# Kernel optimization log

Measured on AMD Instinct MI355X. Metric: run time of the kernel, lower is better.

## Reference

```python
import jax, jax.numpy as jnp
import numpy as np

N = 100000      # nodes
E = 1600000     # edges
DIN = 128       # input_dim
DH = 128        # hidden_dim
DOUT = 64       # output_dim
NL = 10         # num_label_layers


def setup_inputs() -> dict:
    key = jax.random.key(0)
    ks = jax.random.split(key, 12)
    x = jax.random.normal(ks[0], (N, DIN), jnp.float32)
    y = jax.random.uniform(ks[1], (N, DOUT), jnp.float32)
    edge_index = jax.random.randint(ks[2], (2, E), 0, N, dtype=jnp.int32)
    s1 = 1.0 / np.sqrt(DIN)
    s2 = 1.0 / np.sqrt(DH)
    s3 = 1.0 / np.sqrt(DOUT)
    sf = 1.0 / np.sqrt(DH + DOUT)
    Wg1 = jax.random.normal(ks[3], (DIN, DH), jnp.float32) * s1
    bg1 = jnp.zeros((DH,), jnp.float32)
    Wg2 = jax.random.normal(ks[4], (DH, DH), jnp.float32) * s2
    bg2 = jnp.zeros((DH,), jnp.float32)
    Wl = jax.random.normal(ks[5], (NL, DOUT, DOUT), jnp.float32) * s3
    bl = jnp.zeros((NL, DOUT), jnp.float32)
    Wf = jax.random.normal(ks[6], (DH + DOUT, DOUT), jnp.float32) * sf
    bf = jnp.zeros((DOUT,), jnp.float32)
    return {"x": x, "y": y, "edge_index": edge_index,
            "Wg1": Wg1, "bg1": bg1, "Wg2": Wg2, "bg2": bg2,
            "Wl": Wl, "bl": bl, "Wf": Wf, "bf": bf}


def _gcn_conv(h, W, b, src, dst, norm):
    # PyG GCNConv: x' = D^-1/2 (A+I) D^-1/2 (X W) + b
    h = h @ W                                   # [N, dout]
    msg = h[src] * norm[:, None]                # gather + scale: [E+N, dout]
    out = jax.ops.segment_sum(msg, dst, num_segments=N)
    return out + b


def reference(x, y, edge_index, Wg1, bg1, Wg2, bg2, Wl, bl, Wf, bf):
    loops = jnp.arange(N, dtype=edge_index.dtype)
    src = jnp.concatenate([edge_index[0], loops])   # with self-loops
    dst = jnp.concatenate([edge_index[1], loops])
    deg = jax.ops.segment_sum(jnp.ones(dst.shape, jnp.float32), dst, num_segments=N)
    dinv = jnp.where(deg > 0, jax.lax.rsqrt(deg), 0.0)
    norm = dinv[src] * dinv[dst]                    # symmetric GCN normalization

    # GCN feature branch (ReLU between, not after last)
    h = jax.nn.relu(_gcn_conv(x, Wg1, bg1, src, dst, norm))
    h = _gcn_conv(h, Wg2, bg2, src, dst, norm)

    # Label propagation branch
    xl = y
    for j in range(NL):
        xl = _gcn_conv(xl, Wl[j], bl[j], src, dst, norm)
        if j != NL - 1:
            xl = jax.nn.relu(xl)

    fused = jnp.concatenate([h, xl], axis=1) @ Wf + bf
    return jax.nn.sigmoid(fused)
```

## Files before the change

kernel.cpp:

```cpp
#include <hip/hip_runtime.h>
#include <math.h>

#define NN 100000
#define NE 1600000
#define NB 782
#define BCAP 3072
#define BKBLK 128
#define BKCHUNK (NE / BKBLK)
#define DBINS 64

typedef unsigned short ushort_t;
typedef unsigned int uint_t;
typedef __attribute__((ext_vector_type(8))) short bf16x8;
typedef __attribute__((ext_vector_type(8))) unsigned short u16x8;
typedef __attribute__((ext_vector_type(4))) float f32x4;

__device__ __forceinline__ ushort_t f2bf(float f) {
  uint_t u = __float_as_uint(f);
  u = (u + 0x7fffu + ((u >> 16) & 1u)) >> 16;
  return (ushort_t)u;
}
__device__ __forceinline__ float bf2f(ushort_t h) {
  return __uint_as_float((uint_t)h << 16);
}


__global__ __launch_bounds__(512) void bucketA_k(const int* __restrict__ src, const int* __restrict__ dst,
                                                 int* __restrict__ bcnt, uint_t* __restrict__ pairs) {
  __shared__ int h[NB];
  const int t = threadIdx.x;
  const int e0 = blockIdx.x * BKCHUNK;
  for (int b = t; b < NB; b += 512) h[b] = 0;
  __syncthreads();
  for (int i = t; i < BKCHUNK; i += 512) atomicAdd(&h[dst[e0 + i] >> 7], 1);
  __syncthreads();
  for (int b = t; b < NB; b += 512) h[b] = atomicAdd(&bcnt[b], h[b]);
  __syncthreads();
  for (int i = t; i < BKCHUNK; i += 512) {
    int s = src[e0 + i], d = dst[e0 + i];
    int b = d >> 7;
    int pos = atomicAdd(&h[b], 1);
    if (pos < BCAP) pairs[b * BCAP + pos] = ((uint_t)s << 7) | (uint_t)(d & 127);
  }
}

__global__ __launch_bounds__(256) void count2_k(const int* __restrict__ bcnt, const uint_t* __restrict__ pairs,
                                                int* __restrict__ cnt, float* __restrict__ dinv,
                                                int* __restrict__ dbin) {
  __shared__ int c[128];
  __shared__ int hb[DBINS];
  int b = blockIdx.x, t = threadIdx.x;
  if (t < 128) c[t] = 0;
  if (t >= 128 && t < 128 + DBINS) hb[t - 128] = 0;
  __syncthreads();
  int n = min(bcnt[b], BCAP);
  for (int i = t; i < n; i += 256) atomicAdd(&c[pairs[b * BCAP + i] & 127], 1);
  __syncthreads();
  if (t < 128) {
    int node = b * 128 + t;
    if (node < NN) {
      int cc = c[t];
      cnt[node] = cc;
      dinv[node] = rsqrtf((float)(cc + 1));
      atomicAdd(&hb[min(cc, DBINS - 1)], 1);
    }
  }
  __syncthreads();
  if (t < DBINS && hb[t]) atomicAdd(&dbin[t], hb[t]);
}

__global__ __launch_bounds__(1024) void scan1(const int* __restrict__ cnt, int* __restrict__ rowstart,
                                              int* __restrict__ blocksum) {
  __shared__ int s[1024];
  int t = threadIdx.x;
  int i = blockIdx.x * 1024 + t;
  int v = (i < NN) ? cnt[i] : 0;
  s[t] = v;
  __syncthreads();
  for (int off = 1; off < 1024; off <<= 1) {
    int add = (t >= off) ? s[t - off] : 0;
    __syncthreads();
    s[t] += add;
    __syncthreads();
  }
  if (i < NN) rowstart[i] = s[t] - v;
  if (t == 1023) blocksum[blockIdx.x] = s[1023];
}

__global__ void scan2(int* blocksum, int nb, const int* __restrict__ dbin, int* __restrict__ dcur) {
  if (threadIdx.x == 0 && blockIdx.x == 0) {
    int acc = 0;
    for (int b = 0; b < nb; ++b) { int v = blocksum[b]; blocksum[b] = acc; acc += v; }
    int a2 = 0;
    for (int b = 0; b < DBINS; ++b) { dcur[b] = a2; a2 += dbin[b]; }
  }
}

__global__ __launch_bounds__(1024) void scan3(int* __restrict__ rowstart, const int* __restrict__ blocksum) {
  int i = blockIdx.x * 1024 + threadIdx.x;
  if (i < NN) rowstart[i] += blocksum[blockIdx.x];
}

__global__ __launch_bounds__(256) void fillplace_k(const int* __restrict__ bcnt, const uint_t* __restrict__ pairs,
                                                   const int* __restrict__ rowstart, int* __restrict__ csr,
                                                   const int* __restrict__ cnt, int* __restrict__ dcur,
                                                   int* __restrict__ perm) {
  int t = threadIdx.x;
  if (blockIdx.x < NB) {
    __shared__ int cur[128];
    int b = blockIdx.x;
    if (t < 128) cur[t] = 0;
    __syncthreads();
    int n = min(bcnt[b], BCAP);
    for (int i = t; i < n; i += 256) {
      uint_t p = pairs[b * BCAP + i];
      int lo = p & 127;
      int pos = rowstart[b * 128 + lo] + atomicAdd(&cur[lo], 1);
      csr[pos] = (int)(p >> 7);
    }
  } else {
    __shared__ int h[DBINS];
    __shared__ int lbase[DBINS];
    int i = (blockIdx.x - NB) * 256 + t;
    if (t < DBINS) h[t] = 0;
    __syncthreads();
    int bin = 0, lrank = 0;
    if (i < NN) { bin = min(cnt[i], DBINS - 1); lrank = atomicAdd(&h[bin], 1); }
    __syncthreads();
    if (t < DBINS) lbase[t] = h[t] ? atomicAdd(&dcur[t], h[t]) : 0;
    __syncthreads();
    if (i < NN) perm[lbase[bin] + lrank] = i;
  }
}


__global__ __launch_bounds__(256) void wcprep_k(const float* __restrict__ Wg1, const float* __restrict__ Wl,
                                                const float* __restrict__ W2, const float* __restrict__ Wf,
                                                const float* __restrict__ b2, const float* __restrict__ b9,
                                                const float* __restrict__ bfb,
                                                ushort_t* __restrict__ G1h, ushort_t* __restrict__ G1l,
                                                ushort_t* __restrict__ Lh, ushort_t* __restrict__ Ll,
                                                ushort_t* __restrict__ Fh, ushort_t* __restrict__ Fl,
                                                float* __restrict__ bc) {
  if (blockIdx.x < 224) {
    int i = blockIdx.x * 256 + threadIdx.x;
    if (i >= 57344) return;
    float w;
    ushort_t *ph, *pl;
    size_t di;
    if (i < 16384) {
      int k = i >> 7, n = i & 127;
      w = Wg1[i]; di = (size_t)n * 128 + k; ph = G1h; pl = G1l;
    } else {
      int i2 = i - 16384;
      int j = i2 >> 12, r = i2 & 4095;
      int k = r >> 6, n = r & 63;
      w = Wl[i2]; di = (size_t)j * 4096 + n * 64 + k; ph = Lh; pl = Ll;
    }
    ushort_t h = f2bf(w);
    ph[di] = h;
    pl[di] = f2bf(w - bf2f(h));
  } else {
    const float* W9 = Wl + (size_t)9 * 4096;
    int i = (blockIdx.x - 224) * 256 + threadIdx.x;
    if (i >= 12288) return;
    int k = i >> 6, n = i & 63;
    float acc = 0.0f;
    if (k < 128) {
      for (int j = 0; j < 128; ++j) acc += W2[k * 128 + j] * Wf[j * 64 + n];
    } else {
      int k2 = k - 128;
      for (int j = 0; j < 64; ++j) acc += W9[k2 * 64 + j] * Wf[(128 + j) * 64 + n];
    }
    ushort_t h = f2bf(acc);
    Fh[(size_t)n * 192 + k] = h;
    Fl[(size_t)n * 192 + k] = f2bf(acc - bf2f(h));
    if (k == 0) {
      float b = bfb[n];
      for (int j = 0; j < 128; ++j) b += b2[j] * Wf[j * 64 + n];
      for (int j = 0; j < 64; ++j) b += b9[j] * Wf[(128 + j) * 64 + n];
      bc[n] = b;
    }
  }
}


template <int K, int DC>
__global__ __launch_bounds__(256) void mgemm_k(const float* __restrict__ A,
                                               const ushort_t* __restrict__ Wth, const ushort_t* __restrict__ Wtl,
                                               const float* __restrict__ dinv, ushort_t* __restrict__ C) {
  constexpr int NCH = K / 64;
  __shared__ ushort_t Ah[64 * 64], Al[64 * 64];
  __shared__ ushort_t Wh[DC * 64], Wl_[DC * 64];
  const int t = threadIdx.x;
  const int row0 = blockIdx.x * 64;
  const int w = t >> 6, l = t & 63;
  const int lr = l & 15, kh = l >> 4;

  f32x4 acc[DC / 16];
  const f32x4 zz = {0.f, 0.f, 0.f, 0.f};
#pragma unroll
  for (int ct = 0; ct < DC / 16; ++ct) acc[ct] = zz;

  for (int kc = 0; kc < NCH; ++kc) {
    if (kc) __syncthreads();
#pragma unroll
    for (int it = 0; it < 4; ++it) {
      int idx = t + it * 256;
      int row = idx >> 4, kq = idx & 15;
      int gr = min(row0 + row, NN - 1);
      float4 a = *(const float4*)&A[(size_t)gr * K + kc * 64 + kq * 4];
      ushort4 h, lo;
      h.x = f2bf(a.x); lo.x = f2bf(a.x - bf2f(h.x));
      h.y = f2bf(a.y); lo.y = f2bf(a.y - bf2f(h.y));
      h.z = f2bf(a.z); lo.z = f2bf(a.z - bf2f(h.z));
      h.w = f2bf(a.w); lo.w = f2bf(a.w - bf2f(h.w));
      int byt = (row * 128 + kq * 8) ^ ((row & 7) << 4);
      *(ushort4*)&Ah[byt >> 1] = h;
      *(ushort4*)&Al[byt >> 1] = lo;
    }
    for (int idx = t; idx < DC * 8; idx += 256) {
      int n = idx >> 3, kq = idx & 7;
      u16x8 hv = *(const u16x8*)&Wth[(size_t)n * K + kc * 64 + kq * 8];
      u16x8 lv = *(const u16x8*)&Wtl[(size_t)n * K + kc * 64 + kq * 8];
      int byt = (n * 128 + kq * 16) ^ ((n & 7) << 4);
      *(u16x8*)&Wh[byt >> 1] = hv;
      *(u16x8*)&Wl_[byt >> 1] = lv;
    }
    __syncthreads();
#pragma unroll
    for (int kc2 = 0; kc2 < 2; ++kc2) {
      int arow = w * 16 + lr;
      int ab = (arow * 128 + kc2 * 64 + kh * 16) ^ ((arow & 7) << 4);
      bf16x8 ah = *(const bf16x8*)&Ah[ab >> 1];
      bf16x8 al = *(const bf16x8*)&Al[ab >> 1];
#pragma unroll
      for (int ct = 0; ct < DC / 16; ++ct) {
        int n = ct * 16 + lr;
        int bb = (n * 128 + kc2 * 64 + kh * 16) ^ ((n & 7) << 4);
        bf16x8 bh = *(const bf16x8*)&Wh[bb >> 1];
        bf16x8 bl = *(const bf16x8*)&Wl_[bb >> 1];
        acc[ct] = __builtin_amdgcn_mfma_f32_16x16x32_bf16(al, bh, acc[ct], 0, 0, 0);
        acc[ct] = __builtin_amdgcn_mfma_f32_16x16x32_bf16(ah, bl, acc[ct], 0, 0, 0);
        acc[ct] = __builtin_amdgcn_mfma_f32_16x16x32_bf16(ah, bh, acc[ct], 0, 0, 0);
      }
    }
  }
  float dv[4];
#pragma unroll
  for (int r = 0; r < 4; ++r) {
    int grow = row0 + w * 16 + kh * 4 + r;
    dv[r] = (grow < NN) ? dinv[grow] : 0.0f;
  }
#pragma unroll
  for (int ct = 0; ct < DC / 16; ++ct) {
    int col = ct * 16 + lr;
#pragma unroll
    for (int r = 0; r < 4; ++r) {
      int grow = row0 + w * 16 + kh * 4 + r;
      if (grow < NN) C[(size_t)grow * DC + col] = f2bf(acc[ct][r] * dv[r]);
    }
  }
}


template <int K1, int K2, int DC, bool AF32>
__global__ __launch_bounds__(256) void mgemmW_k(const void* __restrict__ A1v, const void* __restrict__ A2v,
                                                const ushort_t* __restrict__ Wth, const ushort_t* __restrict__ Wtl,
                                                const float* __restrict__ dinv, ushort_t* __restrict__ C) {
  constexpr int K = K1 + K2;
  __shared__ ushort_t Wh[DC * K], Wl_[DC * K];
  const int t = threadIdx.x;
  const int w = t >> 6, l = t & 63;
  const int lr = l & 15, kh = l >> 4;
  const int row0 = blockIdx.x * 64;
  const int arow = min(row0 + w * 16 + lr, NN - 1);

  for (int idx = t; idx < DC * (K / 8); idx += 256) {
    int n = idx / (K / 8), kq = idx % (K / 8);
    u16x8 hv = *(const u16x8*)&Wth[(size_t)n * K + kq * 8];
    u16x8 lv = *(const u16x8*)&Wtl[(size_t)n * K + kq * 8];
    int byt = (n * K * 2 + kq * 16) ^ ((n & 7) << 4);
    *(u16x8*)&Wh[byt >> 1] = hv;
    *(u16x8*)&Wl_[byt >> 1] = lv;
  }
  __syncthreads();

  f32x4 acc[DC / 16];
  const f32x4 zz = {0.f, 0.f, 0.f, 0.f};
#pragma unroll
  for (int ct = 0; ct < DC / 16; ++ct) acc[ct] = zz;

#pragma unroll
  for (int kc = 0; kc < K / 32; ++kc) {
    const int kbase = kc * 32 + kh * 8;
    bf16x8 ah, al;
    if constexpr (AF32) {
      const float* Ap;
      if (K2 > 0 && kbase >= K1) Ap = &((const float*)A2v)[(size_t)arow * K2 + kbase - K1];
      else                       Ap = &((const float*)A1v)[(size_t)arow * K1 + kbase];
      float4 a0 = *(const float4*)Ap;
      float4 a1 = *(const float4*)(Ap + 4);
      float av[8] = {a0.x, a0.y, a0.z, a0.w, a1.x, a1.y, a1.z, a1.w};
      u16x8 hv, lv;
#pragma unroll
      for (int e = 0; e < 8; ++e) {
        ushort_t h = f2bf(av[e]);
        hv[e] = h;
        lv[e] = f2bf(av[e] - bf2f(h));
      }
      ah = (bf16x8)hv; al = (bf16x8)lv;
    } else {
      const ushort_t* Ap;
      if (K2 > 0 && kbase >= K1) Ap = &((const ushort_t*)A2v)[(size_t)arow * K2 + kbase - K1];
      else                       Ap = &((const ushort_t*)A1v)[(size_t)arow * K1 + kbase];
      ah = *(const bf16x8*)Ap;
    }
#pragma unroll
    for (int ct = 0; ct < DC / 16; ++ct) {
      const int n = ct * 16 + lr;
      const int bb = (n * K * 2 + kc * 64 + kh * 16) ^ ((n & 7) << 4);
      bf16x8 bh = *(const bf16x8*)&Wh[bb >> 1];
      bf16x8 bl = *(const bf16x8*)&Wl_[bb >> 1];
      if constexpr (AF32) acc[ct] = __builtin_amdgcn_mfma_f32_16x16x32_bf16(al, bh, acc[ct], 0, 0, 0);
      acc[ct] = __builtin_amdgcn_mfma_f32_16x16x32_bf16(ah, bl, acc[ct], 0, 0, 0);
      acc[ct] = __builtin_amdgcn_mfma_f32_16x16x32_bf16(ah, bh, acc[ct], 0, 0, 0);
    }
  }

  float dv[4];
#pragma unroll
  for (int r = 0; r < 4; ++r) {
    int grow = row0 + w * 16 + kh * 4 + r;
    dv[r] = (grow < NN) ? dinv[grow] : 0.0f;
  }
#pragma unroll
  for (int ct = 0; ct < DC / 16; ++ct) {
    int col = ct * 16 + lr;
#pragma unroll
    for (int r = 0; r < 4; ++r) {
      int grow = row0 + w * 16 + kh * 4 + r;
      if (grow < NN) C[(size_t)grow * DC + col] = f2bf(acc[ct][r] * dv[r]);
    }
  }
}


__global__ __launch_bounds__(256) void flay_k(const uint4* __restrict__ U,
                                              const ushort_t* __restrict__ Wth, const ushort_t* __restrict__ Wtl,
                                              const int* __restrict__ perm, const int* __restrict__ rowstart,
                                              const int* __restrict__ cnt, const int* __restrict__ csr,
                                              const float* __restrict__ dinv, const float* __restrict__ bias,
                                              ushort_t* __restrict__ Un) {
  __shared__ ushort_t Wh[64 * 64], Wl_[64 * 64];
  const int t = threadIdx.x;
  for (int idx = t; idx < 64 * 8; idx += 256) {
    int n = idx >> 3, kq = idx & 7;
    u16x8 hv = *(const u16x8*)&Wth[(size_t)n * 64 + kq * 8];
    u16x8 lv = *(const u16x8*)&Wtl[(size_t)n * 64 + kq * 8];
    int byt = (n * 128 + kq * 16) ^ ((n & 7) << 4);
    *(u16x8*)&Wh[byt >> 1] = hv;
    *(u16x8*)&Wl_[byt >> 1] = lv;
  }
  __syncthreads();

  const int w = t >> 6, l = t & 63;
  const int lr = l & 15, kh = l >> 4;
  const int slot0 = blockIdx.x * 64 + w * 16;
  const int slot = min(slot0 + lr, NN - 1);
  const int node = perm[NN - 1 - slot];

  float acc[16];
  {
    uint4 a = U[(size_t)node * 8 + kh];
    uint4 b = U[(size_t)node * 8 + 4 + kh];
    uint_t ua[4] = {a.x, a.y, a.z, a.w};
    uint_t ub[4] = {b.x, b.y, b.z, b.w};
#pragma unroll
    for (int q = 0; q < 4; ++q) {
      acc[2 * q]      = __uint_as_float(ua[q] << 16);
      acc[2 * q + 1]  = __uint_as_float(ua[q] & 0xffff0000u);
      acc[8 + 2 * q]     = __uint_as_float(ub[q] << 16);
      acc[8 + 2 * q + 1] = __uint_as_float(ub[q] & 0xffff0000u);
    }
  }
  int s = rowstart[node], c = cnt[node];
  int j = 0;
  for (; j + 4 <= c; j += 4) {
    int idx[4];
#pragma unroll
    for (int u = 0; u < 4; ++u) idx[u] = csr[s + j + u];
    uint4 va[4], vb[4];
#pragma unroll
    for (int u = 0; u < 4; ++u) {
      va[u] = U[(size_t)idx[u] * 8 + kh];
      vb[u] = U[(size_t)idx[u] * 8 + 4 + kh];
    }
#pragma unroll
    for (int u = 0; u < 4; ++u) {
      uint_t a0 = va[u].x, a1 = va[u].y, a2 = va[u].z, a3 = va[u].w;
      uint_t b0 = vb[u].x, b1 = vb[u].y, b2 = vb[u].z, b3 = vb[u].w;
      acc[0] += __uint_as_float(a0 << 16); acc[1] += __uint_as_float(a0 & 0xffff0000u);
      acc[2] += __uint_as_float(a1 << 16); acc[3] += __uint_as_float(a1 & 0xffff0000u);
      acc[4] += __uint_as_float(a2 << 16); acc[5] += __uint_as_float(a2 & 0xffff0000u);
      acc[6] += __uint_as_float(a3 << 16); acc[7] += __uint_as_float(a3 & 0xffff0000u);
      acc[8]  += __uint_as_float(b0 << 16); acc[9]  += __uint_as_float(b0 & 0xffff0000u);
      acc[10] += __uint_as_float(b1 << 16); acc[11] += __uint_as_float(b1 & 0xffff0000u);
      acc[12] += __uint_as_float(b2 << 16); acc[13] += __uint_as_float(b2 & 0xffff0000u);
      acc[14] += __uint_as_float(b3 << 16); acc[15] += __uint_as_float(b3 & 0xffff0000u);
    }
  }
  for (; j < c; ++j) {
    int sn = csr[s + j];
    uint4 a = U[(size_t)sn * 8 + kh];
    uint4 b = U[(size_t)sn * 8 + 4 + kh];
    uint_t a0 = a.x, a1 = a.y, a2 = a.z, a3 = a.w;
    uint_t b0 = b.x, b1 = b.y, b2 = b.z, b3 = b.w;
    acc[0] += __uint_as_float(a0 << 16); acc[1] += __uint_as_float(a0 & 0xffff0000u);
    acc[2] += __uint_as_float(a1 << 16); acc[3] += __uint_as_float(a1 & 0xffff0000u);
    acc[4] += __uint_as_float(a2 << 16); acc[5] += __uint_as_float(a2 & 0xffff0000u);
    acc[6] += __uint_as_float(a3 << 16); acc[7] += __uint_as_float(a3 & 0xffff0000u);
    acc[8]  += __uint_as_float(b0 << 16); acc[9]  += __uint_as_float(b0 & 0xffff0000u);
    acc[10] += __uint_as_float(b1 << 16); acc[11] += __uint_as_float(b1 & 0xffff0000u);
    acc[12] += __uint_as_float(b2 << 16); acc[13] += __uint_as_float(b2 & 0xffff0000u);
    acc[14] += __uint_as_float(b3 << 16); acc[15] += __uint_as_float(b3 & 0xffff0000u);
  }

  const float dv = dinv[node];
  u16x8 pav, pbv;
#pragma unroll
  for (int q = 0; q < 8; ++q) {
    pav[q] = f2bf(fmaxf(acc[q] * dv + bias[kh * 8 + q], 0.0f));
    pbv[q] = f2bf(fmaxf(acc[8 + q] * dv + bias[32 + kh * 8 + q], 0.0f));
  }
  const bf16x8 pa = (bf16x8)pav, pb = (bf16x8)pbv;

  f32x4 gac[4];
  const f32x4 zz = {0.f, 0.f, 0.f, 0.f};
#pragma unroll
  for (int ct = 0; ct < 4; ++ct) gac[ct] = zz;
#pragma unroll
  for (int ct = 0; ct < 4; ++ct) {
    const int n = ct * 16 + lr;
    const int bb0 = (n * 128 + kh * 16) ^ ((n & 7) << 4);
    const int bb1 = (n * 128 + 64 + kh * 16) ^ ((n & 7) << 4);
    bf16x8 bh0 = *(const bf16x8*)&Wh[bb0 >> 1];
    bf16x8 bl0 = *(const bf16x8*)&Wl_[bb0 >> 1];
    bf16x8 bh1 = *(const bf16x8*)&Wh[bb1 >> 1];
    bf16x8 bl1 = *(const bf16x8*)&Wl_[bb1 >> 1];
    gac[ct] = __builtin_amdgcn_mfma_f32_16x16x32_bf16(pa, bl0, gac[ct], 0, 0, 0);
    gac[ct] = __builtin_amdgcn_mfma_f32_16x16x32_bf16(pa, bh0, gac[ct], 0, 0, 0);
    gac[ct] = __builtin_amdgcn_mfma_f32_16x16x32_bf16(pb, bl1, gac[ct], 0, 0, 0);
    gac[ct] = __builtin_amdgcn_mfma_f32_16x16x32_bf16(pb, bh1, gac[ct], 0, 0, 0);
  }

#pragma unroll
  for (int r = 0; r < 4; ++r) {
    int oslot = slot0 + kh * 4 + r;
    if (oslot < NN) {
      int onode = perm[NN - 1 - oslot];
      float odv = dinv[onode];
#pragma unroll
      for (int ct = 0; ct < 4; ++ct)
        Un[(size_t)onode * 64 + ct * 16 + lr] = f2bf(gac[ct][r] * odv);
    }
  }
}


template <int D, int MODE>
__global__ __launch_bounds__(256) void agg_k(const uint4* __restrict__ t, const int* __restrict__ perm,
                                             const int* __restrict__ rowstart, const int* __restrict__ cnt,
                                             const int* __restrict__ csr, const float* __restrict__ dinv,
                                             const float* __restrict__ bias, void* __restrict__ outv) {
  constexpr int LPN = D / 8;
  int slot = blockIdx.x * (256 / LPN) + threadIdx.x / LPN;
  int lane = threadIdx.x % LPN;
  if (slot >= NN) return;
  int node = perm[NN - 1 - slot];

  float acc[8];
  uint4 sv = t[(size_t)node * LPN + lane];
  {
    uint_t u[4] = {sv.x, sv.y, sv.z, sv.w};
#pragma unroll
    for (int q = 0; q < 4; ++q) {
      acc[2 * q]     = __uint_as_float(u[q] << 16);
      acc[2 * q + 1] = __uint_as_float(u[q] & 0xffff0000u);
    }
  }
  int s = rowstart[node], c = cnt[node];
  int j = 0;
  for (; j + 8 <= c; j += 8) {
    int idx[8];
#pragma unroll
    for (int u = 0; u < 8; ++u) idx[u] = csr[s + j + u];
    uint4 v[8];
#pragma unroll
    for (int u = 0; u < 8; ++u) v[u] = t[(size_t)idx[u] * LPN + lane];
#pragma unroll
    for (int u = 0; u < 8; ++u) {
      uint_t q0 = v[u].x, q1 = v[u].y, q2 = v[u].z, q3 = v[u].w;
      acc[0] += __uint_as_float(q0 << 16); acc[1] += __uint_as_float(q0 & 0xffff0000u);
      acc[2] += __uint_as_float(q1 << 16); acc[3] += __uint_as_float(q1 & 0xffff0000u);
      acc[4] += __uint_as_float(q2 << 16); acc[5] += __uint_as_float(q2 & 0xffff0000u);
      acc[6] += __uint_as_float(q3 << 16); acc[7] += __uint_as_float(q3 & 0xffff0000u);
    }
  }
  for (; j < c; ++j) {
    int sn = csr[s + j];
    uint4 v = t[(size_t)sn * LPN + lane];
    uint_t q0 = v.x, q1 = v.y, q2 = v.z, q3 = v.w;
    acc[0] += __uint_as_float(q0 << 16); acc[1] += __uint_as_float(q0 & 0xffff0000u);
    acc[2] += __uint_as_float(q1 << 16); acc[3] += __uint_as_float(q1 & 0xffff0000u);
    acc[4] += __uint_as_float(q2 << 16); acc[5] += __uint_as_float(q2 & 0xffff0000u);
    acc[6] += __uint_as_float(q3 << 16); acc[7] += __uint_as_float(q3 & 0xffff0000u);
  }
  float dv = dinv[node];
  if constexpr (MODE == 0) {
    u16x8 ov;
#pragma unroll
    for (int q = 0; q < 8; ++q) {
      float o = fmaxf(acc[q] * dv + bias[lane * 8 + q], 0.0f);
      ov[q] = f2bf(o);
    }
    *(u16x8*)&((ushort_t*)outv)[(size_t)node * D + lane * 8] = ov;
  } else {
    float o[8];
#pragma unroll
    for (int q = 0; q < 8; ++q) {
      float v2 = acc[q] * dv + bias[lane * 8 + q];
      o[q] = 1.0f / (1.0f + __expf(-v2));
    }
    float4 o0 = {o[0], o[1], o[2], o[3]};
    float4 o1 = {o[4], o[5], o[6], o[7]};
    float* outf = (float*)outv;
    *(float4*)&outf[(size_t)node * D + lane * 8] = o0;
    *(float4*)&outf[(size_t)node * D + lane * 8 + 4] = o1;
  }
}


extern "C" void kernel_launch(void* const* d_in, const int* in_sizes, int n_in,
                              void* d_out, int out_size, void* d_ws, size_t ws_size,
                              hipStream_t stream) {
  const float* x  = (const float*)d_in[0];
  const float* y  = (const float*)d_in[1];
  const int* ei   = (const int*)d_in[2];
  const float* Wg1 = (const float*)d_in[3];
  const float* bg1 = (const float*)d_in[4];
  const float* Wg2 = (const float*)d_in[5];
  const float* bg2 = (const float*)d_in[6];
  const float* Wl  = (const float*)d_in[7];
  const float* bl  = (const float*)d_in[8];
  const float* Wf  = (const float*)d_in[9];
  const float* bf  = (const float*)d_in[10];
  float* out = (float*)d_out;

  char* ws = (char*)d_ws;
  size_t off = 0;
  auto alloc = [&](size_t bytes) { void* p = ws + off; off += (bytes + 511) & ~(size_t)511; return p; };
  int* cnt      = (int*)alloc((size_t)NN * 4);
  int* rowstart = (int*)alloc((size_t)NN * 4);
  int* blocksum = (int*)alloc(512);
  float* dinv   = (float*)alloc((size_t)NN * 4);
  int* csr      = (int*)alloc((size_t)NE * 4);
  int* bcnt     = (int*)alloc((size_t)NB * 4);
  uint_t* pairs = (uint_t*)alloc((size_t)NB * BCAP * 4);
  int* perm     = (int*)alloc((size_t)NN * 4);
  int* dbin     = (int*)alloc(DBINS * 4);
  int* dcur     = (int*)alloc(DBINS * 4);
  ushort_t* Tb  = (ushort_t*)alloc((size_t)NN * 128 * 2);
  ushort_t* H   = (ushort_t*)alloc((size_t)NN * 128 * 2);
  ushort_t* Ub  = (ushort_t*)alloc((size_t)NN * 64 * 2);
  ushort_t* G1h = (ushort_t*)alloc(128 * 128 * 2);
  ushort_t* G1l = (ushort_t*)alloc(128 * 128 * 2);
  ushort_t* Lh  = (ushort_t*)alloc(10 * 64 * 64 * 2);
  ushort_t* Ll  = (ushort_t*)alloc(10 * 64 * 64 * 2);
  ushort_t* Fh  = (ushort_t*)alloc(64 * 192 * 2);
  ushort_t* Fl  = (ushort_t*)alloc(64 * 192 * 2);
  float* bc     = (float*)alloc(64 * 4);
  ushort_t* uA = Tb;
  ushort_t* uB = Tb + (size_t)NN * 64;

  const int* esrc = ei;
  const int* edst = ei + NE;

  wcprep_k<<<272, 256, 0, stream>>>(Wg1, Wl, Wg2, Wf, bg2, bl + (size_t)9 * 64, bf,
                                    G1h, G1l, Lh, Ll, Fh, Fl, bc);
  hipMemsetAsync(bcnt, 0, (size_t)NB * 4, stream);
  hipMemsetAsync(dbin, 0, DBINS * 4, stream);
  bucketA_k<<<BKBLK, 512, 0, stream>>>(esrc, edst, bcnt, pairs);
  count2_k<<<NB, 256, 0, stream>>>(bcnt, pairs, cnt, dinv, dbin);
  scan1<<<98, 1024, 0, stream>>>(cnt, rowstart, blocksum);
  scan2<<<1, 1, 0, stream>>>(blocksum, 98, dbin, dcur);
  scan3<<<98, 1024, 0, stream>>>(rowstart, blocksum);
  fillplace_k<<<NB + (NN + 255) / 256, 256, 0, stream>>>(bcnt, pairs, rowstart, csr, cnt, dcur, perm);

  const int GG = (NN + 63) / 64;

  mgemm_k<128, 128><<<GG, 256, 0, stream>>>(x, G1h, G1l, dinv, Tb);
  agg_k<128, 0><<<NN / 16, 256, 0, stream>>>((const uint4*)Tb, perm, rowstart, cnt, csr, dinv, bg1, H);

  mgemmW_k<64, 0, 64, true><<<GG, 256, 0, stream>>>(y, nullptr, Lh, Ll, dinv, uA);
  const ushort_t* uin = uA;
  for (int j = 0; j < 8; ++j) {
    ushort_t* uout = (j & 1) ? uA : uB;
    flay_k<<<GG, 256, 0, stream>>>((const uint4*)uin, Lh + (size_t)(j + 1) * 4096, Ll + (size_t)(j + 1) * 4096,
                                   perm, rowstart, cnt, csr, dinv, bl + (size_t)j * 64, uout);
    uin = uout;
  }
  agg_k<64, 0><<<NN / 32, 256, 0, stream>>>((const uint4*)uin, perm, rowstart, cnt, csr, dinv,
                                            bl + (size_t)8 * 64, Ub);

  mgemmW_k<128, 64, 64, false><<<GG, 256, 0, stream>>>(H, Ub, Fh, Fl, dinv, uB);
  agg_k<64, 1><<<NN / 32, 256, 0, stream>>>((const uint4*)uB, perm, rowstart, cnt, csr, dinv, bc, out);
}
```

Measured before the change: 620.8 us.

## Fuse first-layer aggregation and last label aggregation into final linear projection

Replaces the 128-wide GCN aggregation that wrote H, plus the separate final fused GEMM, with two fused kernels. fcv_k aggregates Tb, applies bias and ReLU, and multiplies by the first 128 rows of Wf with MFMA, writing a 64-wide partial. ftail_k aggregates the label branch, applies ReLU, multiplies by the remaining Wf rows and adds the partial. This removes the H buffer write and read and one kernel launch. It also merges the two memsets by placing dbin next to bcnt, and it raises register pressure in the gather loops.

```diff
diff --git a/kernel.cpp b/kernel.cpp
--- a/kernel.cpp
+++ b/kernel.cpp
@@ -468,6 +468,243 @@
 }
 
 
+__global__ __launch_bounds__(512) void fcv_k(const uint4* __restrict__ U,
+                                             const ushort_t* __restrict__ Fh, const ushort_t* __restrict__ Fl,
+                                             const int* __restrict__ perm, const int* __restrict__ rowstart,
+                                             const int* __restrict__ cnt, const int* __restrict__ csr,
+                                             const float* __restrict__ dinv, const float* __restrict__ bias,
+                                             ushort_t* __restrict__ hc) {
+  __shared__ ushort_t Wh[64 * 128], Wl_[64 * 128];
+  const int t = threadIdx.x;
+  for (int idx = t; idx < 64 * 16; idx += 512) {
+    int n = idx >> 4, kq = idx & 15;
+    u16x8 hv = *(const u16x8*)&Fh[(size_t)n * 192 + kq * 8];
+    u16x8 lv = *(const u16x8*)&Fl[(size_t)n * 192 + kq * 8];
+    int byt = (n * 256 + kq * 16) ^ ((n & 7) << 4);
+    *(u16x8*)&Wh[byt >> 1] = hv;
+    *(u16x8*)&Wl_[byt >> 1] = lv;
+  }
+  __syncthreads();
+
+  const int w = t >> 6, l = t & 63;
+  const int lr = l & 15, kh = l >> 4;
+  const int slot0 = blockIdx.x * 128 + w * 16;
+  const int slot = min(slot0 + lr, NN - 1);
+  const int node = perm[NN - 1 - slot];
+
+  float acc[4][8];
+#pragma unroll
+  for (int kc = 0; kc < 4; ++kc) {
+    uint4 v = U[(size_t)node * 16 + kc * 4 + kh];
+    uint_t u[4] = {v.x, v.y, v.z, v.w};
+#pragma unroll
+    for (int q = 0; q < 4; ++q) {
+      acc[kc][2 * q]     = __uint_as_float(u[q] << 16);
+      acc[kc][2 * q + 1] = __uint_as_float(u[q] & 0xffff0000u);
+    }
+  }
+  int s = rowstart[node], c = cnt[node];
+  int j = 0;
+  for (; j + 2 <= c; j += 2) {
+    int i0 = csr[s + j], i1 = csr[s + j + 1];
+    uint4 v0[4], v1[4];
+#pragma unroll
+    for (int kc = 0; kc < 4; ++kc) {
+      v0[kc] = U[(size_t)i0 * 16 + kc * 4 + kh];
+      v1[kc] = U[(size_t)i1 * 16 + kc * 4 + kh];
+    }
+#pragma unroll
+    for (int kc = 0; kc < 4; ++kc) {
+      uint_t u0[4] = {v0[kc].x, v0[kc].y, v0[kc].z, v0[kc].w};
+      uint_t u1[4] = {v1[kc].x, v1[kc].y, v1[kc].z, v1[kc].w};
+#pragma unroll
+      for (int q = 0; q < 4; ++q) {
+        acc[kc][2 * q]     += __uint_as_float(u0[q] << 16) + __uint_as_float(u1[q] << 16);
+        acc[kc][2 * q + 1] += __uint_as_float(u0[q] & 0xffff0000u) + __uint_as_float(u1[q] & 0xffff0000u);
+      }
+    }
+  }
+  for (; j < c; ++j) {
+    int sn = csr[s + j];
+#pragma unroll
+    for (int kc = 0; kc < 4; ++kc) {
+      uint4 v = U[(size_t)sn * 16 + kc * 4 + kh];
+      uint_t u[4] = {v.x, v.y, v.z, v.w};
+#pragma unroll
+      for (int q = 0; q < 4; ++q) {
+        acc[kc][2 * q]     += __uint_as_float(u[q] << 16);
+        acc[kc][2 * q + 1] += __uint_as_float(u[q] & 0xffff0000u);
+      }
+    }
+  }
+
+  const float dv = dinv[node];
+  bf16x8 pa[4];
+#pragma unroll
+  for (int kc = 0; kc < 4; ++kc) {
+    u16x8 pv;
+#pragma unroll
+    for (int q = 0; q < 8; ++q)
+      pv[q] = f2bf(fmaxf(acc[kc][q] * dv + bias[kc * 32 + kh * 8 + q], 0.0f));
+    pa[kc] = (bf16x8)pv;
+  }
+
+  f32x4 gac[4];
+  const f32x4 zz = {0.f, 0.f, 0.f, 0.f};
+#pragma unroll
+  for (int ct = 0; ct < 4; ++ct) gac[ct] = zz;
+#pragma unroll
+  for (int ct = 0; ct < 4; ++ct) {
+    const int n = ct * 16 + lr;
+#pragma unroll
+    for (int kc = 0; kc < 4; ++kc) {
+      const int bb = (n * 256 + kc * 64 + kh * 16) ^ ((n & 7) << 4);
+      bf16x8 bh = *(const bf16x8*)&Wh[bb >> 1];
+      bf16x8 bl = *(const bf16x8*)&Wl_[bb >> 1];
+      gac[ct] = __builtin_amdgcn_mfma_f32_16x16x32_bf16(pa[kc], bl, gac[ct], 0, 0, 0);
+      gac[ct] = __builtin_amdgcn_mfma_f32_16x16x32_bf16(pa[kc], bh, gac[ct], 0, 0, 0);
+    }
+  }
+
+#pragma unroll
+  for (int r = 0; r < 4; ++r) {
+    int oslot = slot0 + kh * 4 + r;
+    if (oslot < NN) {
+      int onode = perm[NN - 1 - oslot];
+      float odv = dinv[onode];
+#pragma unroll
+      for (int ct = 0; ct < 4; ++ct)
+        hc[(size_t)onode * 64 + ct * 16 + lr] = f2bf(gac[ct][r] * odv);
+    }
+  }
+}
+
+
+__global__ __launch_bounds__(256) void ftail_k(const uint4* __restrict__ U,
+                                               const ushort_t* __restrict__ Fh, const ushort_t* __restrict__ Fl,
+                                               const int* __restrict__ perm, const int* __restrict__ rowstart,
+                                               const int* __restrict__ cnt, const int* __restrict__ csr,
+                                               const float* __restrict__ dinv, const float* __restrict__ bias,
+                                               const ushort_t* __restrict__ hc, ushort_t* __restrict__ Un) {
+  __shared__ ushort_t Wh[64 * 64], Wl_[64 * 64];
+  const int t = threadIdx.x;
+  for (int idx = t; idx < 64 * 8; idx += 256) {
+    int n = idx >> 3, kq = idx & 7;
+    u16x8 hv = *(const u16x8*)&Fh[(size_t)n * 192 + 128 + kq * 8];
+    u16x8 lv = *(const u16x8*)&Fl[(size_t)n * 192 + 128 + kq * 8];
+    int byt = (n * 128 + kq * 16) ^ ((n & 7) << 4);
+    *(u16x8*)&Wh[byt >> 1] = hv;
+    *(u16x8*)&Wl_[byt >> 1] = lv;
+  }
+  __syncthreads();
+
+  const int w = t >> 6, l = t & 63;
+  const int lr = l & 15, kh = l >> 4;
+  const int slot0 = blockIdx.x * 64 + w * 16;
+  const int slot = min(slot0 + lr, NN - 1);
+  const int node = perm[NN - 1 - slot];
+
+  float acc[16];
+  {
+    uint4 a = U[(size_t)node * 8 + kh];
+    uint4 b = U[(size_t)node * 8 + 4 + kh];
+    uint_t ua[4] = {a.x, a.y, a.z, a.w};
+    uint_t ub[4] = {b.x, b.y, b.z, b.w};
+#pragma unroll
+    for (int q = 0; q < 4; ++q) {
+      acc[2 * q]      = __uint_as_float(ua[q] << 16);
+      acc[2 * q + 1]  = __uint_as_float(ua[q] & 0xffff0000u);
+      acc[8 + 2 * q]     = __uint_as_float(ub[q] << 16);
+      acc[8 + 2 * q + 1] = __uint_as_float(ub[q] & 0xffff0000u);
+    }
+  }
+  int s = rowstart[node], c = cnt[node];
+  int j = 0;
+  for (; j + 4 <= c; j += 4) {
+    int idx[4];
+#pragma unroll
+    for (int u = 0; u < 4; ++u) idx[u] = csr[s + j + u];
+    uint4 va[4], vb[4];
+#pragma unroll
+    for (int u = 0; u < 4; ++u) {
+      va[u] = U[(size_t)idx[u] * 8 + kh];
+      vb[u] = U[(size_t)idx[u] * 8 + 4 + kh];
+    }
+#pragma unroll
+    for (int u = 0; u < 4; ++u) {
+      uint_t a0 = va[u].x, a1 = va[u].y, a2 = va[u].z, a3 = va[u].w;
+      uint_t b0 = vb[u].x, b1 = vb[u].y, b2 = vb[u].z, b3 = vb[u].w;
+      acc[0] += __uint_as_float(a0 << 16); acc[1] += __uint_as_float(a0 & 0xffff0000u);
+      acc[2] += __uint_as_float(a1 << 16); acc[3] += __uint_as_float(a1 & 0xffff0000u);
+      acc[4] += __uint_as_float(a2 << 16); acc[5] += __uint_as_float(a2 & 0xffff0000u);
+      acc[6] += __uint_as_float(a3 << 16); acc[7] += __uint_as_float(a3 & 0xffff0000u);
+      acc[8]  += __uint_as_float(b0 << 16); acc[9]  += __uint_as_float(b0 & 0xffff0000u);
+      acc[10] += __uint_as_float(b1 << 16); acc[11] += __uint_as_float(b1 & 0xffff0000u);
+      acc[12] += __uint_as_float(b2 << 16); acc[13] += __uint_as_float(b2 & 0xffff0000u);
+      acc[14] += __uint_as_float(b3 << 16); acc[15] += __uint_as_float(b3 & 0xffff0000u);
+    }
+  }
+  for (; j < c; ++j) {
+    int sn = csr[s + j];
+    uint4 a = U[(size_t)sn * 8 + kh];
+    uint4 b = U[(size_t)sn * 8 + 4 + kh];
+    uint_t a0 = a.x, a1 = a.y, a2 = a.z, a3 = a.w;
+    uint_t b0 = b.x, b1 = b.y, b2 = b.z, b3 = b.w;
+    acc[0] += __uint_as_float(a0 << 16); acc[1] += __uint_as_float(a0 & 0xffff0000u);
+    acc[2] += __uint_as_float(a1 << 16); acc[3] += __uint_as_float(a1 & 0xffff0000u);
+    acc[4] += __uint_as_float(a2 << 16); acc[5] += __uint_as_float(a2 & 0xffff0000u);
+    acc[6] += __uint_as_float(a3 << 16); acc[7] += __uint_as_float(a3 & 0xffff0000u);
+    acc[8]  += __uint_as_float(b0 << 16); acc[9]  += __uint_as_float(b0 & 0xffff0000u);
+    acc[10] += __uint_as_float(b1 << 16); acc[11] += __uint_as_float(b1 & 0xffff0000u);
+    acc[12] += __uint_as_float(b2 << 16); acc[13] += __uint_as_float(b2 & 0xffff0000u);
+    acc[14] += __uint_as_float(b3 << 16); acc[15] += __uint_as_float(b3 & 0xffff0000u);
+  }
+
+  const float dv = dinv[node];
+  u16x8 pav, pbv;
+#pragma unroll
+  for (int q = 0; q < 8; ++q) {
+    pav[q] = f2bf(fmaxf(acc[q] * dv + bias[kh * 8 + q], 0.0f));
+    pbv[q] = f2bf(fmaxf(acc[8 + q] * dv + bias[32 + kh * 8 + q], 0.0f));
+  }
+  const bf16x8 pa = (bf16x8)pav, pb = (bf16x8)pbv;
+
+  f32x4 gac[4];
+  const f32x4 zz = {0.f, 0.f, 0.f, 0.f};
+#pragma unroll
+  for (int ct = 0; ct < 4; ++ct) gac[ct] = zz;
+#pragma unroll
+  for (int ct = 0; ct < 4; ++ct) {
+    const int n = ct * 16 + lr;
+    const int bb0 = (n * 128 + kh * 16) ^ ((n & 7) << 4);
+    const int bb1 = (n * 128 + 64 + kh * 16) ^ ((n & 7) << 4);
+    bf16x8 bh0 = *(const bf16x8*)&Wh[bb0 >> 1];
+    bf16x8 bl0 = *(const bf16x8*)&Wl_[bb0 >> 1];
+    bf16x8 bh1 = *(const bf16x8*)&Wh[bb1 >> 1];
+    bf16x8 bl1 = *(const bf16x8*)&Wl_[bb1 >> 1];
+    gac[ct] = __builtin_amdgcn_mfma_f32_16x16x32_bf16(pa, bl0, gac[ct], 0, 0, 0);
+    gac[ct] = __builtin_amdgcn_mfma_f32_16x16x32_bf16(pa, bh0, gac[ct], 0, 0, 0);
+    gac[ct] = __builtin_amdgcn_mfma_f32_16x16x32_bf16(pb, bl1, gac[ct], 0, 0, 0);
+    gac[ct] = __builtin_amdgcn_mfma_f32_16x16x32_bf16(pb, bh1, gac[ct], 0, 0, 0);
+  }
+
+#pragma unroll
+  for (int r = 0; r < 4; ++r) {
+    int oslot = slot0 + kh * 4 + r;
+    if (oslot < NN) {
+      int onode = perm[NN - 1 - oslot];
+      float odv = dinv[onode];
+#pragma unroll
+      for (int ct = 0; ct < 4; ++ct) {
+        int col = ct * 16 + lr;
+        float v = gac[ct][r] * odv + bf2f(hc[(size_t)onode * 64 + col]);
+        Un[(size_t)onode * 64 + col] = f2bf(v);
+      }
+    }
+  }
+}
+
+
 template <int D, int MODE>
 __global__ __launch_bounds__(256) void agg_k(const uint4* __restrict__ t, const int* __restrict__ perm,
                                              const int* __restrict__ rowstart, const int* __restrict__ cnt,
@@ -566,12 +803,11 @@
   float* dinv   = (float*)alloc((size_t)NN * 4);
   int* csr      = (int*)alloc((size_t)NE * 4);
   int* bcnt     = (int*)alloc((size_t)NB * 4);
+  int* dbin     = (int*)alloc(DBINS * 4);
   uint_t* pairs = (uint_t*)alloc((size_t)NB * BCAP * 4);
   int* perm     = (int*)alloc((size_t)NN * 4);
-  int* dbin     = (int*)alloc(DBINS * 4);
   int* dcur     = (int*)alloc(DBINS * 4);
   ushort_t* Tb  = (ushort_t*)alloc((size_t)NN * 128 * 2);
-  ushort_t* H   = (ushort_t*)alloc((size_t)NN * 128 * 2);
   ushort_t* Ub  = (ushort_t*)alloc((size_t)NN * 64 * 2);
   ushort_t* G1h = (ushort_t*)alloc(128 * 128 * 2);
   ushort_t* G1l = (ushort_t*)alloc(128 * 128 * 2);
@@ -588,8 +824,7 @@
 
   wcprep_k<<<272, 256, 0, stream>>>(Wg1, Wl, Wg2, Wf, bg2, bl + (size_t)9 * 64, bf,
                                     G1h, G1l, Lh, Ll, Fh, Fl, bc);
-  hipMemsetAsync(bcnt, 0, (size_t)NB * 4, stream);
-  hipMemsetAsync(dbin, 0, DBINS * 4, stream);
+  hipMemsetAsync(bcnt, 0, 4096, stream);
   bucketA_k<<<BKBLK, 512, 0, stream>>>(esrc, edst, bcnt, pairs);
   count2_k<<<NB, 256, 0, stream>>>(bcnt, pairs, cnt, dinv, dbin);
   scan1<<<98, 1024, 0, stream>>>(cnt, rowstart, blocksum);
@@ -600,7 +835,8 @@
   const int GG = (NN + 63) / 64;
 
   mgemm_k<128, 128><<<GG, 256, 0, stream>>>(x, G1h, G1l, dinv, Tb);
-  agg_k<128, 0><<<NN / 16, 256, 0, stream>>>((const uint4*)Tb, perm, rowstart, cnt, csr, dinv, bg1, H);
+  fcv_k<<<(NN + 127) / 128, 512, 0, stream>>>((const uint4*)Tb, Fh, Fl, perm, rowstart, cnt, csr,
+                                              dinv, bg1, Ub);
 
   mgemmW_k<64, 0, 64, true><<<GG, 256, 0, stream>>>(y, nullptr, Lh, Ll, dinv, uA);
   const ushort_t* uin = uA;
@@ -610,9 +846,8 @@
                                    perm, rowstart, cnt, csr, dinv, bl + (size_t)j * 64, uout);
     uin = uout;
   }
-  agg_k<64, 0><<<NN / 32, 256, 0, stream>>>((const uint4*)uin, perm, rowstart, cnt, csr, dinv,
-                                            bl + (size_t)8 * 64, Ub);
-
-  mgemmW_k<128, 64, 64, false><<<GG, 256, 0, stream>>>(H, Ub, Fh, Fl, dinv, uB);
+  ftail_k<<<GG, 256, 0, stream>>>((const uint4*)uin, Fh, Fl, perm, rowstart, cnt, csr,
+                                  dinv, bl + (size_t)8 * 64, Ub, uB);
+
   agg_k<64, 1><<<NN / 32, 256, 0, stream>>>((const uint4*)uB, perm, rowstart, cnt, csr, dinv, bc, out);
 }
```

New measurement: 615.0 us. No clear change (-0.9%).
